# Performance work log

Measured on AMD Instinct MI355X. Metric: run time of the kernel, lower is better.

Reference implementation:

```python
import jax, jax.numpy as jnp
import numpy as np

N = 100000   # nodes
E = 600000   # edges
G = 512      # graphs in batch
EPS = 1e-5   # LayerNorm eps
IN_DIM = 60 + 2 + 12  # dyn feats*frames + dims + st embedding
H = 128


def setup_inputs() -> dict:
    key = jax.random.key(0)
    ks = jax.random.split(key, 32)
    inp = {
        "x": jax.random.normal(ks[0], (N, 60), jnp.float32),
        "xdims": jax.random.uniform(ks[1], (N, 2), jnp.float32),
        "xsttype": jax.random.randint(ks[2], (N,), 0, 256, jnp.int32),
        "edge_index": jax.random.randint(ks[3], (2, E), 0, N, jnp.int32),
        "batch": jnp.sort(jax.random.randint(ks[4], (N,), 0, G, jnp.int32)),
        "emb": jax.random.normal(ks[5], (256, 12), jnp.float32),
    }
    def lin(k, i, o):
        s = 1.0 / np.sqrt(i)
        return jax.random.uniform(k, (i, o), jnp.float32, -s, s)
    dims = [IN_DIM, H, H]
    for l in range(2):
        i, o = dims[l], dims[l + 1]
        inp[f"Wl{l}"] = lin(ks[6 + 4 * l], i, o)   # lin_l: applied to aggregated neighbors
        inp[f"bl{l}"] = jnp.zeros((o,), jnp.float32)
        inp[f"Wr{l}"] = lin(ks[7 + 4 * l], i, o)   # lin_r: applied to root (no bias, PyG SAGEConv)
        inp[f"g{l}"] = jnp.ones((o,), jnp.float32)   # LayerNorm gamma
        inp[f"bn{l}"] = jnp.zeros((o,), jnp.float32)  # LayerNorm beta
    ld = [2 * H, 50, 50, 10]
    for l in range(3):
        inp[f"Wf{l}"] = lin(ks[20 + l], ld[l], ld[l + 1])
        inp[f"bf{l}"] = jnp.zeros((ld[l + 1],), jnp.float32)
    return inp


def _layer_norm(h, g, b):
    mu = jnp.mean(h, axis=-1, keepdims=True)
    var = jnp.mean(jnp.square(h - mu), axis=-1, keepdims=True)
    return (h - mu) * jax.lax.rsqrt(var + EPS) * g + b


def reference(x, xdims, xsttype, edge_index, batch, emb,
              Wl0, bl0, Wr0, g0, bn0,
              Wl1, bl1, Wr1, g1, bn1,
              Wf0, bf0, Wf1, bf1, Wf2, bf2):
    # node feature assembly: [N, 60+2+12]
    h = jnp.concatenate([x, xdims, emb[xsttype]], axis=1)

    src, dst = edge_index[0], edge_index[1]
    deg = jax.ops.segment_sum(jnp.ones((E,), h.dtype), dst, num_segments=N)
    inv_deg = (1.0 / jnp.maximum(deg, 1.0))[:, None]

    for Wl, bl, Wr, g, bn in ((Wl0, bl0, Wr0, g0, bn0), (Wl1, bl1, Wr1, g1, bn1)):
        # SAGEConv (mean aggr): out = lin_l(mean_j x_j) + lin_r(x_i)
        agg = jax.ops.segment_sum(h[src], dst, num_segments=N) * inv_deg
        h = agg @ Wl + bl + h @ Wr
        h = jax.nn.relu(_layer_norm(h, g, bn))  # dropout inactive (eval)

    # global mean / max pooling over graphs
    cnt = jax.ops.segment_sum(jnp.ones((N,), h.dtype), batch, num_segments=G)
    xmean = jax.ops.segment_sum(h, batch, num_segments=G) / jnp.maximum(cnt, 1.0)[:, None]
    xmax = jax.ops.segment_max(h, batch, num_segments=G)
    z = jnp.concatenate([xmean, xmax], axis=1)  # [G, 2H]

    for Wf, bf in ((Wf0, bf0), (Wf1, bf1), (Wf2, bf2)):
        z = jax.nn.relu(z @ Wf + bf)  # Linear + ReLU + Dropout(eval)
    return z
```

## Files before the change

kernel.cpp:

```cpp
#include <hip/hip_runtime.h>

#define NN 100000
#define NP 100096
#define NT (NP / 32)
#define GB 1024
#define EE 600000
#define GG 512
#define LN_EPS 1e-5f

typedef __attribute__((ext_vector_type(8))) __bf16 bf16x8;
typedef __attribute__((ext_vector_type(4))) float f32x4;

__device__ __forceinline__ unsigned short f2bf(float f) {
    unsigned int u = __float_as_uint(f);
    u = (u + 0x7fffu + ((u >> 16) & 1u)) >> 16;
    return (unsigned short)u;
}
__device__ __forceinline__ unsigned int pack2(float a, float b) {
    return (unsigned int)f2bf(a) | ((unsigned int)f2bf(b) << 16);
}
__device__ __forceinline__ void acc8(float* s, uint4 v) {
    s[0] += __uint_as_float(v.x << 16);
    s[1] += __uint_as_float(v.x & 0xffff0000u);
    s[2] += __uint_as_float(v.y << 16);
    s[3] += __uint_as_float(v.y & 0xffff0000u);
    s[4] += __uint_as_float(v.z << 16);
    s[5] += __uint_as_float(v.z & 0xffff0000u);
    s[6] += __uint_as_float(v.w << 16);
    s[7] += __uint_as_float(v.w & 0xffff0000u);
}

#define PREP_A (NP * 10)
#define PREP_W0 (128 * 160)
#define PREP_W1 (128 * 256)
#define PREP_TOT (PREP_A + PREP_W0 + PREP_W1 + EE)

__global__ __launch_bounds__(256) void prep_kernel(
    const float* __restrict__ x, const float* __restrict__ xdims,
    const int* __restrict__ stt, const float* __restrict__ emb,
    const int* __restrict__ ei,
    const float* __restrict__ Wl0, const float* __restrict__ Wr0,
    const float* __restrict__ Wl1, const float* __restrict__ Wr1,
    unsigned short* __restrict__ H0r,
    unsigned short* __restrict__ Wt0, unsigned short* __restrict__ Wt1,
    int* __restrict__ deg)
{
    int idx = blockIdx.x * 256 + threadIdx.x;
    if (idx < PREP_A) {
        int node = idx / 10;
        int c8 = (idx - node * 10) * 8;
        unsigned short vals[8];
        if (node < NN) {
            int st = stt[node];
            #pragma unroll
            for (int i = 0; i < 8; ++i) {
                int f = c8 + i;
                float v = 0.f;
                if (f < 60)      v = x[node * 60 + f];
                else if (f < 62) v = xdims[node * 2 + (f - 60)];
                else if (f < 74) v = emb[st * 12 + (f - 62)];
                vals[i] = f2bf(v);
            }
        } else {
            #pragma unroll
            for (int i = 0; i < 8; ++i) vals[i] = 0;
        }
        uint4 o;
        o.x = (unsigned)vals[0] | ((unsigned)vals[1] << 16);
        o.y = (unsigned)vals[2] | ((unsigned)vals[3] << 16);
        o.z = (unsigned)vals[4] | ((unsigned)vals[5] << 16);
        o.w = (unsigned)vals[6] | ((unsigned)vals[7] << 16);
        *(uint4*)(H0r + (size_t)node * 80 + c8) = o;
    } else if (idx < PREP_A + PREP_W0) {
        int j = idx - PREP_A;
        int n = j / 160, k = j - n * 160;
        float v = 0.f;
        if (k < 74)                  v = Wl0[k * 128 + n];
        else if (k >= 80 && k < 154) v = Wr0[(k - 80) * 128 + n];
        Wt0[(size_t)n * 160 + k] = f2bf(v);
    } else if (idx < PREP_A + PREP_W0 + PREP_W1) {
        int j = idx - PREP_A - PREP_W0;
        int n = j >> 8, k = j & 255;
        float v = (k < 128) ? Wl1[k * 128 + n] : Wr1[(k - 128) * 128 + n];
        Wt1[(size_t)n * 256 + k] = f2bf(v);
    } else if (idx < PREP_TOT) {
        int e = idx - PREP_A - PREP_W0 - PREP_W1;
        atomicAdd(&deg[ei[EE + e]], 1);
    }
}

__global__ __launch_bounds__(256) void scan1_kernel(
    const int* __restrict__ deg, int* __restrict__ offs, int* __restrict__ bsum)
{
    __shared__ int ts[256];
    int t = threadIdx.x;
    int base = blockIdx.x * 2048 + t * 8;
    int d[8];
    if (base + 8 <= NN) {
        int4 a = *(const int4*)&deg[base];
        int4 b = *(const int4*)&deg[base + 4];
        d[0]=a.x; d[1]=a.y; d[2]=a.z; d[3]=a.w;
        d[4]=b.x; d[5]=b.y; d[6]=b.z; d[7]=b.w;
    } else {
        #pragma unroll
        for (int i = 0; i < 8; ++i) d[i] = (base + i < NN) ? deg[base + i] : 0;
    }
    int e[8]; int run = 0;
    #pragma unroll
    for (int i = 0; i < 8; ++i) { e[i] = run; run += d[i]; }
    ts[t] = run;
    int tot = run;
    __syncthreads();
    for (int off = 1; off < 256; off <<= 1) {
        int u = (t >= off) ? ts[t - off] : 0;
        __syncthreads();
        ts[t] += u;
        __syncthreads();
// ... 16 lines not shown
    if (t < nb) bsum[t] = inc - v;
}

__global__ __launch_bounds__(256) void fill_csr_kernel(
    const int* __restrict__ ei, int* __restrict__ cur,
    const int* __restrict__ offs, const int* __restrict__ bsum,
    int* __restrict__ csr)
{
    int e = blockIdx.x * 256 + threadIdx.x;
    if (e >= EE) return;
    int d = ei[EE + e];
    int p = offs[d] + bsum[d >> 11] + atomicAdd(&cur[d], 1);
    csr[p] = ei[e];
}

__global__ __launch_bounds__(256) void agg0_kernel(
    const unsigned short* __restrict__ H0r, unsigned short* __restrict__ A0g,
    const int* __restrict__ csr, const int* __restrict__ offs,
    const int* __restrict__ bsum, const int* __restrict__ deg)
{
    int node = blockIdx.x * 16 + (threadIdx.x >> 4);
    int lane = threadIdx.x & 15;
    if (node >= NP || lane >= 10) return;
    int d = 0, st = 0;
    if (node < NN) { d = deg[node]; st = offs[node] + bsum[node >> 11]; }
    float iv = 1.0f / (float)(d > 1 ? d : 1);
    float s[8];
    #pragma unroll
    for (int i = 0; i < 8; ++i) s[i] = 0.f;
    int e = 0;
    for (; e + 4 <= d; e += 4) {
        int i0 = csr[st + e],     i1 = csr[st + e + 1];
        int i2 = csr[st + e + 2], i3 = csr[st + e + 3];
        uint4 v0 = *(const uint4*)(H0r + (size_t)i0 * 80 + lane * 8);
        uint4 v1 = *(const uint4*)(H0r + (size_t)i1 * 80 + lane * 8);
        uint4 v2 = *(const uint4*)(H0r + (size_t)i2 * 80 + lane * 8);
        uint4 v3 = *(const uint4*)(H0r + (size_t)i3 * 80 + lane * 8);
        acc8(s, v0); acc8(s, v1); acc8(s, v2); acc8(s, v3);
    }
    for (; e < d; ++e) {
        int i0 = csr[st + e];
        uint4 v0 = *(const uint4*)(H0r + (size_t)i0 * 80 + lane * 8);
        acc8(s, v0);
    }
    uint4 o;
    o.x = pack2(s[0] * iv, s[1] * iv);
    o.y = pack2(s[2] * iv, s[3] * iv);
    o.z = pack2(s[4] * iv, s[5] * iv);
    o.w = pack2(s[6] * iv, s[7] * iv);
    *(uint4*)(A0g + (size_t)node * 80 + lane * 8) = o;
}

__global__ __launch_bounds__(256) void agg1_kernel(
    const unsigned short* __restrict__ H1, unsigned short* __restrict__ A1g,
    const int* __restrict__ csr, const int* __restrict__ offs,
    const int* __restrict__ bsum, const int* __restrict__ deg)
{
    int node = blockIdx.x * 16 + (threadIdx.x >> 4);
    int lane = threadIdx.x & 15;
    if (node >= NP) return;
    int d = 0, st = 0;
    if (node < NN) { d = deg[node]; st = offs[node] + bsum[node >> 11]; }
    float iv = 1.0f / (float)(d > 1 ? d : 1);
    float s[8];
    #pragma unroll
    for (int i = 0; i < 8; ++i) s[i] = 0.f;
    int e = 0;
    for (; e + 4 <= d; e += 4) {
        int i0 = csr[st + e],     i1 = csr[st + e + 1];
        int i2 = csr[st + e + 2], i3 = csr[st + e + 3];
        uint4 v0 = *(const uint4*)(H1 + (size_t)i0 * 128 + lane * 8);
        uint4 v1 = *(const uint4*)(H1 + (size_t)i1 * 128 + lane * 8);
        uint4 v2 = *(const uint4*)(H1 + (size_t)i2 * 128 + lane * 8);
        uint4 v3 = *(const uint4*)(H1 + (size_t)i3 * 128 + lane * 8);
        acc8(s, v0); acc8(s, v1); acc8(s, v2); acc8(s, v3);
    }
    for (; e < d; ++e) {
        int i0 = csr[st + e];
        uint4 v0 = *(const uint4*)(H1 + (size_t)i0 * 128 + lane * 8);
        acc8(s, v0);
    }
    uint4 o;
    o.x = pack2(s[0] * iv, s[1] * iv);
    o.y = pack2(s[2] * iv, s[3] * iv);
    o.z = pack2(s[4] * iv, s[5] * iv);
    o.w = pack2(s[6] * iv, s[7] * iv);
    *(uint4*)(A1g + (size_t)node * 128 + lane * 8) = o;
}

template<int K, bool POOL>
__global__ __launch_bounds__(256, 4) void gemm_kernel(
    const unsigned short* __restrict__ Ag,
    const unsigned short* __restrict__ Hr,
    const unsigned short* __restrict__ Wt,
    const float* __restrict__ bias, const float* __restrict__ gamma,
    const float* __restrict__ beta,
    unsigned short* __restrict__ outH,
    const int* __restrict__ batch,
    float* __restrict__ psum, int* __restrict__ pmax)
{
    constexpr int KT = K / 32, AS = K + 8, CPR = K / 8, CPRh = CPR / 2, RH = K / 2;
    constexpr int SMEM = (32 * AS * 2 > 32 * 128 * 4) ? 32 * AS * 2 : 32 * 128 * 4;
    __shared__ __align__(16) char smem[SMEM];
    unsigned short* Asm = (unsigned short*)smem;
    float* Hs = (float*)smem;
    __shared__ __align__(16) float sP[32 * 4];
    __shared__ __align__(16) float qP[32 * 4];
    __shared__ int bS[32];

    const int tid = threadIdx.x;
    const int l = tid & 63, w = tid >> 6;
    const int g = l >> 4, c0 = l & 15;

    bf16x8 bfr[KT][2];
    #pragma unroll
    for (int j = 0; j < 2; ++j) {
        const unsigned short* bp = Wt + (size_t)((2 * w + j) * 16 + c0) * K + g * 8;
        #pragma unroll
        for (int kt = 0; kt < KT; ++kt)
            bfr[kt][j] = *(const bf16x8*)(bp + kt * 32);
    }
    float bia[2], gam[2], bet[2];
    #pragma unroll
    for (int j = 0; j < 2; ++j) {
        int col = (2 * w + j) * 16 + c0;
        bia[j] = bias[col]; gam[j] = gamma[col]; bet[j] = beta[col];
    }
    const unsigned short* ar0 = Asm + (0 * 16 + c0) * AS + g * 8;
    const unsigned short* ar1 = Asm + (1 * 16 + c0) * AS + g * 8;

    for (int t = blockIdx.x; t < NT; t += gridDim.x) {
        const int n0 = t * 32;
        if (POOL && tid < 32) {
            int gn = n0 + tid;
            bS[tid] = (gn < NN) ? batch[gn] : -1;
        }
        for (int i = tid; i < 32 * CPR; i += 256) {
            int node = i / CPR, c = i - node * CPR;
            size_t gn = (size_t)(n0 + node);
            const unsigned short* src = (c < CPRh)
                ? (Ag + gn * RH + c * 8)
                : (Hr + gn * RH + (c - CPRh) * 8);
            uint4 v = *(const uint4*)src;
            *(uint4*)(Asm + node * AS + c * 8) = v;
        }
        __syncthreads();

        f32x4 acc[2][2];
        acc[0][0] = (f32x4){0.f,0.f,0.f,0.f}; acc[0][1] = (f32x4){0.f,0.f,0.f,0.f};
        acc[1][0] = (f32x4){0.f,0.f,0.f,0.f}; acc[1][1] = (f32x4){0.f,0.f,0.f,0.f};
        #pragma unroll
        for (int kt = 0; kt < KT; ++kt) {
            bf16x8 a0 = *(const bf16x8*)(ar0 + kt * 32);
            bf16x8 a1 = *(const bf16x8*)(ar1 + kt * 32);
            acc[0][0] = __builtin_amdgcn_mfma_f32_16x16x32_bf16(a0, bfr[kt][0], acc[0][0], 0, 0, 0);
            acc[0][1] = __builtin_amdgcn_mfma_f32_16x16x32_bf16(a0, bfr[kt][1], acc[0][1], 0, 0, 0);
            acc[1][0] = __builtin_amdgcn_mfma_f32_16x16x32_bf16(a1, bfr[kt][0], acc[1][0], 0, 0, 0);
            acc[1][1] = __builtin_amdgcn_mfma_f32_16x16x32_bf16(a1, bfr[kt][1], acc[1][1], 0, 0, 0);
        }

        #pragma unroll
        for (int m = 0; m < 2; ++m) {
            #pragma unroll
            for (int r = 0; r < 4; ++r) {
                float h0v = acc[m][0][r] + bia[0];
                float h1v = acc[m][1][r] + bia[1];
                float s = h0v + h1v, q = h0v * h0v + h1v * h1v;
                #pragma unroll
                for (int mm = 1; mm < 16; mm <<= 1) {
                    s += __shfl_xor(s, mm, 64);
                    q += __shfl_xor(q, mm, 64);
                }
                if (c0 == 0) {
                    int node = m * 16 + g * 4 + r;
                    sP[node * 4 + w] = s;
                    qP[node * 4 + w] = q;
                }
            }
        }
        __syncthreads();

        #pragma unroll
        for (int m = 0; m < 2; ++m) {
            #pragma unroll
            for (int r = 0; r < 4; ++r) {
                int node = m * 16 + g * 4 + r;
                float4 sv = *(const float4*)&sP[node * 4];
                float4 qv = *(const float4*)&qP[node * 4];
                float s = (sv.x + sv.y) + (sv.z + sv.w);
                float q = (qv.x + qv.y) + (qv.z + qv.w);
                float mu   = s * (1.f / 128.f);
                float var  = q * (1.f / 128.f) - mu * mu;
                float rinv = rsqrtf(var + LN_EPS);
                float h0v = acc[m][0][r] + bia[0];
                float h1v = acc[m][1][r] + bia[1];
                float v0 = fmaxf(0.f, (h0v - mu) * rinv * gam[0] + bet[0]);
                float v1 = fmaxf(0.f, (h1v - mu) * rinv * gam[1] + bet[1]);
                if (POOL) {
                    Hs[node * 128 + (2 * w) * 16 + c0]     = v0;
                    Hs[node * 128 + (2 * w + 1) * 16 + c0] = v1;
                } else {
                    size_t gn = (size_t)(n0 + node);
                    outH[gn * 128 + (2 * w) * 16 + c0]     = f2bf(v0);
                    outH[gn * 128 + (2 * w + 1) * 16 + c0] = f2bf(v1);
                }
            }
        }
        __syncthreads();

        if (POOL) {
            if (tid < 128) {
                int j = tid;
                int curg = -1; float s = 0.f, m = 0.f;
                #pragma unroll 4
                for (int n = 0; n < 32; ++n) {
                    int gb = bS[n];
                    if (gb < 0) break;
                    if (gb != curg) {
                        if (curg >= 0) {
                            atomicAdd(&psum[curg * 128 + j], s);
                            atomicMax(&pmax[curg * 128 + j], __float_as_int(m));
                        }
                        curg = gb; s = 0.f; m = 0.f;
                    }
                    float v = Hs[n * 128 + j];
                    s += v; m = fmaxf(m, v);
                }
                if (curg >= 0) {
                    atomicAdd(&psum[curg * 128 + j], s);
                    atomicMax(&pmax[curg * 128 + j], __float_as_int(m));
                }
            }
            __syncthreads();
        }
    }
}

__device__ __forceinline__ int lbound(const int* a, int n, int v) {
    int lo = 0, hi = n;
    while (lo < hi) { int mid = (lo + hi) >> 1; if (a[mid] < v) lo = mid + 1; else hi = mid; }
    return lo;
}

__global__ __launch_bounds__(64) void mlp_kernel(
    const float* __restrict__ psum, const int* __restrict__ pmax,
    const int* __restrict__ batch,
    const float* __restrict__ Wf0, const float* __restrict__ bf0,
    const float* __restrict__ Wf1, const float* __restrict__ bf1,
    const float* __restrict__ Wf2, const float* __restrict__ bf2,
    float* __restrict__ out)
{
    __shared__ float z[256];
    __shared__ float t1[50];
    __shared__ float t2[50];
    __shared__ int cS;
    int g = blockIdx.x, t = threadIdx.x;
    if (t == 0) cS = lbound(batch, NN, g + 1) - lbound(batch, NN, g);
    __syncthreads();
    int c = cS;
    float ic = 1.0f / (float)(c > 1 ? c : 1);
    for (int j = t; j < 128; j += 64) {
        z[j]       = psum[g * 128 + j] * ic;
        z[128 + j] = __int_as_float(pmax[g * 128 + j]);
    }
    __syncthreads();
    if (t < 50) {
// ... 13 lines not shown
        for (int k = 0; k < 50; ++k) a = fmaf(t2[k], Wf2[k * 10 + t], a);
        out[g * 10 + t] = fmaxf(a, 0.0f);
    }
}

extern "C" void kernel_launch(void* const* d_in, const int* in_sizes, int n_in,
                              void* d_out, int out_size, void* d_ws, size_t ws_size,
                              hipStream_t stream)
{
    const float* x     = (const float*)d_in[0];
    const float* xdims = (const float*)d_in[1];
    const int*   stt   = (const int*)d_in[2];
    const int*   ei    = (const int*)d_in[3];
    const int*   batch = (const int*)d_in[4];
    const float* emb   = (const float*)d_in[5];
    const float* Wl0   = (const float*)d_in[6];
    const float* bl0   = (const float*)d_in[7];
    const float* Wr0   = (const float*)d_in[8];
    const float* g0    = (const float*)d_in[9];
    const float* bn0   = (const float*)d_in[10];
    const float* Wl1   = (const float*)d_in[11];
    const float* bl1   = (const float*)d_in[12];
    const float* Wr1   = (const float*)d_in[13];
    const float* g1    = (const float*)d_in[14];
    const float* bn1   = (const float*)d_in[15];
    const float* Wf0   = (const float*)d_in[16];
    const float* bf0   = (const float*)d_in[17];
    const float* Wf1   = (const float*)d_in[18];
    const float* bf1   = (const float*)d_in[19];
    const float* Wf2   = (const float*)d_in[20];
    const float* bf2   = (const float*)d_in[21];

    char* w = (char*)d_ws;
    unsigned short* H0r = (unsigned short*)w; w += (size_t)NP * 80 * 2;
    unsigned short* A0g = (unsigned short*)w; w += (size_t)NP * 80 * 2;
    unsigned short* H1  = (unsigned short*)w; w += (size_t)NP * 128 * 2;
    unsigned short* A1g = (unsigned short*)w; w += (size_t)NP * 128 * 2;
    unsigned short* Wt0 = (unsigned short*)w; w += (size_t)128 * 160 * 2;
    unsigned short* Wt1 = (unsigned short*)w; w += (size_t)128 * 256 * 2;
    int*   csr    = (int*)w;   w += (size_t)EE * 4;
    int*   offs   = (int*)w;   w += (size_t)NN * 4;
    int*   bsum   = (int*)w;   w += 1024;
    char* zbeg = w;
    int*   deg  = (int*)w;   w += (size_t)NP * 4;
    int*   cur  = (int*)w;   w += (size_t)NN * 4;
    float* psum = (float*)w; w += (size_t)GG * 128 * 4;
    int*   pmax = (int*)w;   w += (size_t)GG * 128 * 4;
    size_t zsz = (size_t)(w - zbeg);

    hipMemsetAsync(zbeg, 0, zsz, stream);

    prep_kernel<<<(PREP_TOT + 255) / 256, 256, 0, stream>>>(
        x, xdims, stt, emb, ei, Wl0, Wr0, Wl1, Wr1, H0r, Wt0, Wt1, deg);

    int nb = (NN + 2047) / 2048;
    scan1_kernel<<<nb, 256, 0, stream>>>(deg, offs, bsum);
    scan2_kernel<<<1, 64, 0, stream>>>(bsum, nb);
    fill_csr_kernel<<<(EE + 255) / 256, 256, 0, stream>>>(ei, cur, offs, bsum, csr);

    agg0_kernel<<<NP / 16, 256, 0, stream>>>(H0r, A0g, csr, offs, bsum, deg);
    gemm_kernel<160, false><<<GB, 256, 0, stream>>>(
        A0g, H0r, Wt0, bl0, g0, bn0, H1, nullptr, nullptr, nullptr);
    agg1_kernel<<<NP / 16, 256, 0, stream>>>(H1, A1g, csr, offs, bsum, deg);
    gemm_kernel<256, true><<<GB, 256, 0, stream>>>(
        A1g, H1, Wt1, bl1, g1, bn1, nullptr, batch, psum, pmax);

    mlp_kernel<<<GG, 64, 0, stream>>>(psum, pmax, batch, Wf0, bf0, Wf1, bf1, Wf2, bf2,
                                      (float*)d_out);
}
```

Measured before the change: 329.9 us.

## Load GEMM operands directly from global memory, one 32-node tile per block

The fused SAGE GEMM+LayerNorm kernel drops its persistent-block loop and LDS staging of the activation tile. Each block now handles one 32-node tile, with every wave loading its A and W fragments straight from global memory in groups of four k-steps, then issuing the MFMAs. This removes a shared-memory round trip and a barrier per tile, and lets more blocks be resident. The cost is that each wave reloads weight fragments per tile instead of keeping them in registers across tiles, and all four waves load the same A rows redundantly.

```diff
diff --git a/kernel.cpp b/kernel.cpp
--- a/kernel.cpp
+++ b/kernel.cpp
@@ -3,7 +3,6 @@
 #define NN 100000
 #define NP 100096
 #define NT (NP / 32)
-#define GB 1024
 #define EE 600000
 #define GG 512
 #define LN_EPS 1e-5f
@@ -222,7 +221,7 @@
 }
 
 template<int K, bool POOL>
-__global__ __launch_bounds__(256, 4) void gemm_kernel(
+__global__ __launch_bounds__(256) void gemm_kernel(
     const unsigned short* __restrict__ Ag,
     const unsigned short* __restrict__ Hr,
     const unsigned short* __restrict__ Wt,
@@ -232,139 +231,139 @@
     const int* __restrict__ batch,
     float* __restrict__ psum, int* __restrict__ pmax)
 {
-    constexpr int KT = K / 32, AS = K + 8, CPR = K / 8, CPRh = CPR / 2, RH = K / 2;
-    constexpr int SMEM = (32 * AS * 2 > 32 * 128 * 4) ? 32 * AS * 2 : 32 * 128 * 4;
-    __shared__ __align__(16) char smem[SMEM];
-    unsigned short* Asm = (unsigned short*)smem;
-    float* Hs = (float*)smem;
+    constexpr int KT = K / 32, KH = K / 2;
     __shared__ __align__(16) float sP[32 * 4];
     __shared__ __align__(16) float qP[32 * 4];
-    __shared__ int bS[32];
+    __shared__ __align__(16) float Hs[POOL ? 32 * 128 : 4];
+    __shared__ int bS[POOL ? 32 : 1];
 
     const int tid = threadIdx.x;
+    const int n0 = blockIdx.x * 32;
     const int l = tid & 63, w = tid >> 6;
     const int g = l >> 4, c0 = l & 15;
 
-    bf16x8 bfr[KT][2];
-    #pragma unroll
-    for (int j = 0; j < 2; ++j) {
-        const unsigned short* bp = Wt + (size_t)((2 * w + j) * 16 + c0) * K + g * 8;
-        #pragma unroll
-        for (int kt = 0; kt < KT; ++kt)
-            bfr[kt][j] = *(const bf16x8*)(bp + kt * 32);
-    }
+    if (POOL && tid < 32) {
+        int gn = n0 + tid;
+        bS[tid] = (gn < NN) ? batch[gn] : -1;
+    }
+
+    const unsigned short* ag0 = Ag + (size_t)(n0 + c0) * KH;
+    const unsigned short* hr0 = Hr + (size_t)(n0 + c0) * KH;
+    const unsigned short* ag1 = Ag + (size_t)(n0 + 16 + c0) * KH;
+    const unsigned short* hr1 = Hr + (size_t)(n0 + 16 + c0) * KH;
+    const unsigned short* bp0 = Wt + (size_t)((2 * w + 0) * 16 + c0) * K + g * 8;
+    const unsigned short* bp1 = Wt + (size_t)((2 * w + 1) * 16 + c0) * K + g * 8;
+
     float bia[2], gam[2], bet[2];
     #pragma unroll
     for (int j = 0; j < 2; ++j) {
         int col = (2 * w + j) * 16 + c0;
         bia[j] = bias[col]; gam[j] = gamma[col]; bet[j] = beta[col];
     }
-    const unsigned short* ar0 = Asm + (0 * 16 + c0) * AS + g * 8;
-    const unsigned short* ar1 = Asm + (1 * 16 + c0) * AS + g * 8;
-
-    for (int t = blockIdx.x; t < NT; t += gridDim.x) {
-        const int n0 = t * 32;
-        if (POOL && tid < 32) {
-            int gn = n0 + tid;
-            bS[tid] = (gn < NN) ? batch[gn] : -1;
-        }
-        for (int i = tid; i < 32 * CPR; i += 256) {
-            int node = i / CPR, c = i - node * CPR;
-            size_t gn = (size_t)(n0 + node);
-            const unsigned short* src = (c < CPRh)
-                ? (Ag + gn * RH + c * 8)
-                : (Hr + gn * RH + (c - CPRh) * 8);
-            uint4 v = *(const uint4*)src;
-            *(uint4*)(Asm + node * AS + c * 8) = v;
-        }
-        __syncthreads();
-
-        f32x4 acc[2][2];
-        acc[0][0] = (f32x4){0.f,0.f,0.f,0.f}; acc[0][1] = (f32x4){0.f,0.f,0.f,0.f};
-        acc[1][0] = (f32x4){0.f,0.f,0.f,0.f}; acc[1][1] = (f32x4){0.f,0.f,0.f,0.f};
+
+    f32x4 acc[2][2];
+    acc[0][0] = (f32x4){0.f,0.f,0.f,0.f}; acc[0][1] = (f32x4){0.f,0.f,0.f,0.f};
+    acc[1][0] = (f32x4){0.f,0.f,0.f,0.f}; acc[1][1] = (f32x4){0.f,0.f,0.f,0.f};
+
+    #pragma unroll
+    for (int kb = 0; kb < KT; kb += 4) {
+        constexpr int NB = 4;
+        const int nb = (KT - kb < NB) ? (KT - kb) : NB;
+        bf16x8 bfr[NB][2], afr[NB][2];
         #pragma unroll
-        for (int kt = 0; kt < KT; ++kt) {
-            bf16x8 a0 = *(const bf16x8*)(ar0 + kt * 32);
-            bf16x8 a1 = *(const bf16x8*)(ar1 + kt * 32);
-            acc[0][0] = __builtin_amdgcn_mfma_f32_16x16x32_bf16(a0, bfr[kt][0], acc[0][0], 0, 0, 0);
-            acc[0][1] = __builtin_amdgcn_mfma_f32_16x16x32_bf16(a0, bfr[kt][1], acc[0][1], 0, 0, 0);
-            acc[1][0] = __builtin_amdgcn_mfma_f32_16x16x32_bf16(a1, bfr[kt][0], acc[1][0], 0, 0, 0);
-            acc[1][1] = __builtin_amdgcn_mfma_f32_16x16x32_bf16(a1, bfr[kt][1], acc[1][1], 0, 0, 0);
-        }
-
+        for (int kk = 0; kk < NB; ++kk) {
+            if (kk < nb) {
+                int kt = kb + kk;
+                int c = kt * 32 + g * 8;
+                bfr[kk][0] = *(const bf16x8*)(bp0 + kt * 32);
+                bfr[kk][1] = *(const bf16x8*)(bp1 + kt * 32);
+                const unsigned short* a0p = (c < KH) ? (ag0 + c) : (hr0 + c - KH);
+                const unsigned short* a1p = (c < KH) ? (ag1 + c) : (hr1 + c - KH);
+                afr[kk][0] = *(const bf16x8*)a0p;
+                afr[kk][1] = *(const bf16x8*)a1p;
+            }
+        }
         #pragma unroll
-        for (int m = 0; m < 2; ++m) {
+        for (int kk = 0; kk < NB; ++kk) {
+            if (kk < nb) {
+                acc[0][0] = __builtin_amdgcn_mfma_f32_16x16x32_bf16(afr[kk][0], bfr[kk][0], acc[0][0], 0, 0, 0);
+                acc[0][1] = __builtin_amdgcn_mfma_f32_16x16x32_bf16(afr[kk][0], bfr[kk][1], acc[0][1], 0, 0, 0);
+                acc[1][0] = __builtin_amdgcn_mfma_f32_16x16x32_bf16(afr[kk][1], bfr[kk][0], acc[1][0], 0, 0, 0);
+                acc[1][1] = __builtin_amdgcn_mfma_f32_16x16x32_bf16(afr[kk][1], bfr[kk][1], acc[1][1], 0, 0, 0);
+            }
+        }
+    }
+
+    #pragma unroll
+    for (int m = 0; m < 2; ++m) {
+        #pragma unroll
+        for (int r = 0; r < 4; ++r) {
+            float h0v = acc[m][0][r] + bia[0];
+            float h1v = acc[m][1][r] + bia[1];
+            float s = h0v + h1v, q = h0v * h0v + h1v * h1v;
             #pragma unroll
-            for (int r = 0; r < 4; ++r) {
-                float h0v = acc[m][0][r] + bia[0];
-                float h1v = acc[m][1][r] + bia[1];
-                float s = h0v + h1v, q = h0v * h0v + h1v * h1v;
-                #pragma unroll
-                for (int mm = 1; mm < 16; mm <<= 1) {
-                    s += __shfl_xor(s, mm, 64);
-                    q += __shfl_xor(q, mm, 64);
-                }
-                if (c0 == 0) {
-                    int node = m * 16 + g * 4 + r;
-                    sP[node * 4 + w] = s;
-                    qP[node * 4 + w] = q;
-                }
-            }
-        }
-        __syncthreads();
-
+            for (int mm = 1; mm < 16; mm <<= 1) {
+                s += __shfl_xor(s, mm, 64);
+                q += __shfl_xor(q, mm, 64);
+            }
+            if (c0 == 0) {
+                int node = m * 16 + g * 4 + r;
+                sP[node * 4 + w] = s;
+                qP[node * 4 + w] = q;
+            }
+        }
+    }
+    __syncthreads();
+
+    #pragma unroll
+    for (int m = 0; m < 2; ++m) {
         #pragma unroll
-        for (int m = 0; m < 2; ++m) {
-            #pragma unroll
-            for (int r = 0; r < 4; ++r) {
-                int node = m * 16 + g * 4 + r;
-                float4 sv = *(const float4*)&sP[node * 4];
-                float4 qv = *(const float4*)&qP[node * 4];
-                float s = (sv.x + sv.y) + (sv.z + sv.w);
-                float q = (qv.x + qv.y) + (qv.z + qv.w);
-                float mu   = s * (1.f / 128.f);
-                float var  = q * (1.f / 128.f) - mu * mu;
-                float rinv = rsqrtf(var + LN_EPS);
-                float h0v = acc[m][0][r] + bia[0];
-                float h1v = acc[m][1][r] + bia[1];
-                float v0 = fmaxf(0.f, (h0v - mu) * rinv * gam[0] + bet[0]);
-                float v1 = fmaxf(0.f, (h1v - mu) * rinv * gam[1] + bet[1]);
-                if (POOL) {
-                    Hs[node * 128 + (2 * w) * 16 + c0]     = v0;
-                    Hs[node * 128 + (2 * w + 1) * 16 + c0] = v1;
-                } else {
-                    size_t gn = (size_t)(n0 + node);
-                    outH[gn * 128 + (2 * w) * 16 + c0]     = f2bf(v0);
-                    outH[gn * 128 + (2 * w + 1) * 16 + c0] = f2bf(v1);
-                }
-            }
-        }
-        __syncthreads();
-
-        if (POOL) {
-            if (tid < 128) {
-                int j = tid;
-                int curg = -1; float s = 0.f, m = 0.f;
-                #pragma unroll 4
-                for (int n = 0; n < 32; ++n) {
-                    int gb = bS[n];
-                    if (gb < 0) break;
-                    if (gb != curg) {
-                        if (curg >= 0) {
-                            atomicAdd(&psum[curg * 128 + j], s);
-                            atomicMax(&pmax[curg * 128 + j], __float_as_int(m));
-                        }
-                        curg = gb; s = 0.f; m = 0.f;
-                    }
-                    float v = Hs[n * 128 + j];
-                    s += v; m = fmaxf(m, v);
-                }
+        for (int r = 0; r < 4; ++r) {
+            int node = m * 16 + g * 4 + r;
+            float4 sv = *(const float4*)&sP[node * 4];
+            float4 qv = *(const float4*)&qP[node * 4];
+            float s = (sv.x + sv.y) + (sv.z + sv.w);
+            float q = (qv.x + qv.y) + (qv.z + qv.w);
+            float mu   = s * (1.f / 128.f);
+            float var  = q * (1.f / 128.f) - mu * mu;
+            float rinv = rsqrtf(var + LN_EPS);
+            float h0v = acc[m][0][r] + bia[0];
+            float h1v = acc[m][1][r] + bia[1];
+            float v0 = fmaxf(0.f, (h0v - mu) * rinv * gam[0] + bet[0]);
+            float v1 = fmaxf(0.f, (h1v - mu) * rinv * gam[1] + bet[1]);
+            if (POOL) {
+                Hs[node * 128 + (2 * w) * 16 + c0]     = v0;
+                Hs[node * 128 + (2 * w + 1) * 16 + c0] = v1;
+            } else {
+                size_t gn = (size_t)(n0 + node);
+                outH[gn * 128 + (2 * w) * 16 + c0]     = f2bf(v0);
+                outH[gn * 128 + (2 * w + 1) * 16 + c0] = f2bf(v1);
+            }
+        }
+    }
+    if (!POOL) return;
+    __syncthreads();
+
+    if (tid < 128) {
+        int j = tid;
+        int curg = -1; float s = 0.f, m = 0.f;
+        #pragma unroll 4
+        for (int n = 0; n < 32; ++n) {
+            int gb = bS[n];
+            if (gb < 0) break;
+            if (gb != curg) {
                 if (curg >= 0) {
                     atomicAdd(&psum[curg * 128 + j], s);
                     atomicMax(&pmax[curg * 128 + j], __float_as_int(m));
                 }
-            }
-            __syncthreads();
+                curg = gb; s = 0.f; m = 0.f;
+            }
+            float v = Hs[n * 128 + j];
+            s += v; m = fmaxf(m, v);
+        }
+        if (curg >= 0) {
+            atomicAdd(&psum[curg * 128 + j], s);
+            atomicMax(&pmax[curg * 128 + j], __float_as_int(m));
         }
     }
 }
@@ -471,10 +470,10 @@
     fill_csr_kernel<<<(EE + 255) / 256, 256, 0, stream>>>(ei, cur, offs, bsum, csr);
 
     agg0_kernel<<<NP / 16, 256, 0, stream>>>(H0r, A0g, csr, offs, bsum, deg);
-    gemm_kernel<160, false><<<GB, 256, 0, stream>>>(
+    gemm_kernel<160, false><<<NT, 256, 0, stream>>>(
         A0g, H0r, Wt0, bl0, g0, bn0, H1, nullptr, nullptr, nullptr);
     agg1_kernel<<<NP / 16, 256, 0, stream>>>(H1, A1g, csr, offs, bsum, deg);
-    gemm_kernel<256, true><<<GB, 256, 0, stream>>>(
+    gemm_kernel<256, true><<<NT, 256, 0, stream>>>(
         A1g, H1, Wt1, bl1, g1, bn1, nullptr, batch, psum, pmax);
 
     mlp_kernel<<<GG, 64, 0, stream>>>(psum, pmax, batch, Wf0, bf0, Wf1, bf1, Wf2, bf2,
```

After: 325.1 us. No clear change (-1.5%).

## Restructure SAGE GEMM: direct global-to-LDS loads, 64-node tiles, padded row strides

Applied to the files above, without the earlier changes.

The GEMM kernels drop the persistent grid-stride loop over 32-node tiles. They now launch one 512-thread block per 64-node tile, and each wave computes a single 16-column slice. The A and H tiles are staged with global_load_lds straight into shared memory, skipping the register round trip. Row strides of the node feature and weight arrays are padded (88/136/168/264) so the tiles copy contiguously and LDS accesses avoid bank conflicts. In exchange, B fragments are no longer held in registers across tiles but reloaded from global memory per block. The padding also enlarges the feature buffers the aggregation kernels read and write.

```diff
diff --git a/kernel.cpp b/kernel.cpp
--- a/kernel.cpp
+++ b/kernel.cpp
@@ -2,11 +2,14 @@
 
 #define NN 100000
 #define NP 100096
-#define NT (NP / 32)
-#define GB 1024
 #define EE 600000
 #define GG 512
 #define LN_EPS 1e-5f
+
+#define PS0 88
+#define PS1 136
+#define SW0 168
+#define SW1 264
 
 typedef __attribute__((ext_vector_type(8))) __bf16 bf16x8;
 typedef __attribute__((ext_vector_type(4))) float f32x4;
@@ -28,6 +31,11 @@
     s[5] += __uint_as_float(v.z & 0xffff0000u);
     s[6] += __uint_as_float(v.w << 16);
     s[7] += __uint_as_float(v.w & 0xffff0000u);
+}
+__device__ __forceinline__ void gl_lds16(const unsigned short* g, unsigned short* l) {
+    __builtin_amdgcn_global_load_lds(
+        (const __attribute__((address_space(1))) void*)g,
+        (__attribute__((address_space(3))) void*)l, 16, 0, 0);
 }
 
 #define PREP_A (NP * 10)
@@ -70,19 +78,19 @@
         o.y = (unsigned)vals[2] | ((unsigned)vals[3] << 16);
         o.z = (unsigned)vals[4] | ((unsigned)vals[5] << 16);
         o.w = (unsigned)vals[6] | ((unsigned)vals[7] << 16);
-        *(uint4*)(H0r + (size_t)node * 80 + c8) = o;
+        *(uint4*)(H0r + (size_t)node * PS0 + c8) = o;
     } else if (idx < PREP_A + PREP_W0) {
         int j = idx - PREP_A;
         int n = j / 160, k = j - n * 160;
         float v = 0.f;
         if (k < 74)                  v = Wl0[k * 128 + n];
         else if (k >= 80 && k < 154) v = Wr0[(k - 80) * 128 + n];
-        Wt0[(size_t)n * 160 + k] = f2bf(v);
+        Wt0[(size_t)n * SW0 + k] = f2bf(v);
     } else if (idx < PREP_A + PREP_W0 + PREP_W1) {
         int j = idx - PREP_A - PREP_W0;
         int n = j >> 8, k = j & 255;
         float v = (k < 128) ? Wl1[k * 128 + n] : Wr1[(k - 128) * 128 + n];
-        Wt1[(size_t)n * 256 + k] = f2bf(v);
+        Wt1[(size_t)n * SW1 + k] = f2bf(v);
     } else if (idx < PREP_TOT) {
         int e = idx - PREP_A - PREP_W0 - PREP_W1;
         atomicAdd(&deg[ei[EE + e]], 1);
@@ -165,15 +173,15 @@
     for (; e + 4 <= d; e += 4) {
         int i0 = csr[st + e],     i1 = csr[st + e + 1];
         int i2 = csr[st + e + 2], i3 = csr[st + e + 3];
-        uint4 v0 = *(const uint4*)(H0r + (size_t)i0 * 80 + lane * 8);
-        uint4 v1 = *(const uint4*)(H0r + (size_t)i1 * 80 + lane * 8);
-        uint4 v2 = *(const uint4*)(H0r + (size_t)i2 * 80 + lane * 8);
-        uint4 v3 = *(const uint4*)(H0r + (size_t)i3 * 80 + lane * 8);
+        uint4 v0 = *(const uint4*)(H0r + (size_t)i0 * PS0 + lane * 8);
+        uint4 v1 = *(const uint4*)(H0r + (size_t)i1 * PS0 + lane * 8);
+        uint4 v2 = *(const uint4*)(H0r + (size_t)i2 * PS0 + lane * 8);
+        uint4 v3 = *(const uint4*)(H0r + (size_t)i3 * PS0 + lane * 8);
         acc8(s, v0); acc8(s, v1); acc8(s, v2); acc8(s, v3);
     }
     for (; e < d; ++e) {
         int i0 = csr[st + e];
-        uint4 v0 = *(const uint4*)(H0r + (size_t)i0 * 80 + lane * 8);
+        uint4 v0 = *(const uint4*)(H0r + (size_t)i0 * PS0 + lane * 8);
         acc8(s, v0);
     }
     uint4 o;
@@ -181,7 +189,7 @@
     o.y = pack2(s[2] * iv, s[3] * iv);
     o.z = pack2(s[4] * iv, s[5] * iv);
     o.w = pack2(s[6] * iv, s[7] * iv);
-    *(uint4*)(A0g + (size_t)node * 80 + lane * 8) = o;
+    *(uint4*)(A0g + (size_t)node * PS0 + lane * 8) = o;
 }
 
 __global__ __launch_bounds__(256) void agg1_kernel(
@@ -202,15 +210,15 @@
     for (; e + 4 <= d; e += 4) {
         int i0 = csr[st + e],     i1 = csr[st + e + 1];
         int i2 = csr[st + e + 2], i3 = csr[st + e + 3];
-        uint4 v0 = *(const uint4*)(H1 + (size_t)i0 * 128 + lane * 8);
-        uint4 v1 = *(const uint4*)(H1 + (size_t)i1 * 128 + lane * 8);
-        uint4 v2 = *(const uint4*)(H1 + (size_t)i2 * 128 + lane * 8);
-        uint4 v3 = *(const uint4*)(H1 + (size_t)i3 * 128 + lane * 8);
+        uint4 v0 = *(const uint4*)(H1 + (size_t)i0 * PS1 + lane * 8);
+        uint4 v1 = *(const uint4*)(H1 + (size_t)i1 * PS1 + lane * 8);
+        uint4 v2 = *(const uint4*)(H1 + (size_t)i2 * PS1 + lane * 8);
+        uint4 v3 = *(const uint4*)(H1 + (size_t)i3 * PS1 + lane * 8);
         acc8(s, v0); acc8(s, v1); acc8(s, v2); acc8(s, v3);
     }
     for (; e < d; ++e) {
         int i0 = csr[st + e];
-        uint4 v0 = *(const uint4*)(H1 + (size_t)i0 * 128 + lane * 8);
+        uint4 v0 = *(const uint4*)(H1 + (size_t)i0 * PS1 + lane * 8);
         acc8(s, v0);
     }
     uint4 o;
@@ -218,11 +226,11 @@
     o.y = pack2(s[2] * iv, s[3] * iv);
     o.z = pack2(s[4] * iv, s[5] * iv);
     o.w = pack2(s[6] * iv, s[7] * iv);
-    *(uint4*)(A1g + (size_t)node * 128 + lane * 8) = o;
-}
-
-template<int K, bool POOL>
-__global__ __launch_bounds__(256, 4) void gemm_kernel(
+    *(uint4*)(A1g + (size_t)node * PS1 + lane * 8) = o;
+}
+
+template<int K, int KH, int PS, int SW, bool POOL>
+__global__ __launch_bounds__(512) void gemm_kernel(
     const unsigned short* __restrict__ Ag,
     const unsigned short* __restrict__ Hr,
     const unsigned short* __restrict__ Wt,
@@ -232,139 +240,128 @@
     const int* __restrict__ batch,
     float* __restrict__ psum, int* __restrict__ pmax)
 {
-    constexpr int KT = K / 32, AS = K + 8, CPR = K / 8, CPRh = CPR / 2, RH = K / 2;
-    constexpr int SMEM = (32 * AS * 2 > 32 * 128 * 4) ? 32 * AS * 2 : 32 * 128 * 4;
-    __shared__ __align__(16) char smem[SMEM];
-    unsigned short* Asm = (unsigned short*)smem;
-    float* Hs = (float*)smem;
-    __shared__ __align__(16) float sP[32 * 4];
-    __shared__ __align__(16) float qP[32 * 4];
-    __shared__ int bS[32];
+    constexpr int KT = K / 32;
+    constexpr int CH = 64 * PS / 8;
+    __shared__ __align__(16) unsigned short ASm[2 * 64 * PS];
+    __shared__ __align__(16) float sP[64 * 8];
+    __shared__ __align__(16) float qP[64 * 8];
+    __shared__ int bS[64];
 
     const int tid = threadIdx.x;
+    const int n0 = blockIdx.x * 64;
     const int l = tid & 63, w = tid >> 6;
     const int g = l >> 4, c0 = l & 15;
 
-    bf16x8 bfr[KT][2];
-    #pragma unroll
-    for (int j = 0; j < 2; ++j) {
-        const unsigned short* bp = Wt + (size_t)((2 * w + j) * 16 + c0) * K + g * 8;
+    if (POOL && tid < 64) {
+        int gn = n0 + tid;
+        bS[tid] = (gn < NN) ? batch[gn] : -1;
+    }
+    {
+        const unsigned short* gA = Ag + (size_t)n0 * PS;
+        const unsigned short* gH = Hr + (size_t)n0 * PS;
+        for (int i = tid; i < 2 * CH; i += 512) {
+            const unsigned short* src = (i < CH) ? (gA + i * 8) : (gH + (i - CH) * 8);
+            unsigned short* dst = ASm + i * 8;
+            gl_lds16(src, dst);
+        }
+    }
+
+    const int col = w * 16 + c0;
+    const unsigned short* bp = Wt + (size_t)col * SW + g * 8;
+    const float bia = bias[col], gam = gamma[col], bet = beta[col];
+
+    __syncthreads();
+
+    f32x4 acc[4];
+    #pragma unroll
+    for (int m = 0; m < 4; ++m) acc[m] = (f32x4){0.f, 0.f, 0.f, 0.f};
+
+    #pragma unroll
+    for (int m = 0; m < 4; ++m) {
+        int node = m * 16 + c0;
+        bf16x8 af[KT], bf[KT];
+        #pragma unroll
+        for (int kt = 0; kt < KT; ++kt) {
+            int k = kt * 32 + g * 8;
+            const unsigned short* ap = (k < KH)
+                ? (ASm + node * PS + k)
+                : (ASm + 64 * PS + node * PS + (k - KH));
+            af[kt] = *(const bf16x8*)ap;
+            bf[kt] = *(const bf16x8*)(bp + kt * 32);
+        }
         #pragma unroll
         for (int kt = 0; kt < KT; ++kt)
-            bfr[kt][j] = *(const bf16x8*)(bp + kt * 32);
-    }
-    float bia[2], gam[2], bet[2];
-    #pragma unroll
-    for (int j = 0; j < 2; ++j) {
-        int col = (2 * w + j) * 16 + c0;
-        bia[j] = bias[col]; gam[j] = gamma[col]; bet[j] = beta[col];
-    }
-    const unsigned short* ar0 = Asm + (0 * 16 + c0) * AS + g * 8;
-    const unsigned short* ar1 = Asm + (1 * 16 + c0) * AS + g * 8;
-
-    for (int t = blockIdx.x; t < NT; t += gridDim.x) {
-        const int n0 = t * 32;
-        if (POOL && tid < 32) {
-            int gn = n0 + tid;
-            bS[tid] = (gn < NN) ? batch[gn] : -1;
-        }
-        for (int i = tid; i < 32 * CPR; i += 256) {
-            int node = i / CPR, c = i - node * CPR;
-            size_t gn = (size_t)(n0 + node);
-            const unsigned short* src = (c < CPRh)
-                ? (Ag + gn * RH + c * 8)
-                : (Hr + gn * RH + (c - CPRh) * 8);
-            uint4 v = *(const uint4*)src;
-            *(uint4*)(Asm + node * AS + c * 8) = v;
-        }
-        __syncthreads();
-
-        f32x4 acc[2][2];
-        acc[0][0] = (f32x4){0.f,0.f,0.f,0.f}; acc[0][1] = (f32x4){0.f,0.f,0.f,0.f};
-        acc[1][0] = (f32x4){0.f,0.f,0.f,0.f}; acc[1][1] = (f32x4){0.f,0.f,0.f,0.f};
+            acc[m] = __builtin_amdgcn_mfma_f32_16x16x32_bf16(af[kt], bf[kt], acc[m], 0, 0, 0);
+    }
+
+    #pragma unroll
+    for (int m = 0; m < 4; ++m) {
         #pragma unroll
-        for (int kt = 0; kt < KT; ++kt) {
-            bf16x8 a0 = *(const bf16x8*)(ar0 + kt * 32);
-            bf16x8 a1 = *(const bf16x8*)(ar1 + kt * 32);
-            acc[0][0] = __builtin_amdgcn_mfma_f32_16x16x32_bf16(a0, bfr[kt][0], acc[0][0], 0, 0, 0);
-            acc[0][1] = __builtin_amdgcn_mfma_f32_16x16x32_bf16(a0, bfr[kt][1], acc[0][1], 0, 0, 0);
-            acc[1][0] = __builtin_amdgcn_mfma_f32_16x16x32_bf16(a1, bfr[kt][0], acc[1][0], 0, 0, 0);
-            acc[1][1] = __builtin_amdgcn_mfma_f32_16x16x32_bf16(a1, bfr[kt][1], acc[1][1], 0, 0, 0);
-        }
-
+        for (int r = 0; r < 4; ++r) {
+            float h = acc[m][r] + bia;
+            float s = h, q = h * h;
+            #pragma unroll
+            for (int mm = 1; mm < 16; mm <<= 1) {
+                s += __shfl_xor(s, mm, 64);
+                q += __shfl_xor(q, mm, 64);
+            }
+            if (c0 == 0) {
+                int node = m * 16 + g * 4 + r;
+                sP[node * 8 + w] = s;
+                qP[node * 8 + w] = q;
+            }
+        }
+    }
+    __syncthreads();
+
+    float* Hs = (float*)ASm;
+
+    #pragma unroll
+    for (int m = 0; m < 4; ++m) {
         #pragma unroll
-        for (int m = 0; m < 2; ++m) {
-            #pragma unroll
-            for (int r = 0; r < 4; ++r) {
-                float h0v = acc[m][0][r] + bia[0];
-                float h1v = acc[m][1][r] + bia[1];
-                float s = h0v + h1v, q = h0v * h0v + h1v * h1v;
-                #pragma unroll
-                for (int mm = 1; mm < 16; mm <<= 1) {
-                    s += __shfl_xor(s, mm, 64);
-                    q += __shfl_xor(q, mm, 64);
-                }
-                if (c0 == 0) {
-                    int node = m * 16 + g * 4 + r;
-                    sP[node * 4 + w] = s;
-                    qP[node * 4 + w] = q;
-                }
+        for (int r = 0; r < 4; ++r) {
+            int node = m * 16 + g * 4 + r;
+            float4 sv0 = *(const float4*)&sP[node * 8];
+            float4 sv1 = *(const float4*)&sP[node * 8 + 4];
+            float4 qv0 = *(const float4*)&qP[node * 8];
+            float4 qv1 = *(const float4*)&qP[node * 8 + 4];
+            float s = ((sv0.x + sv0.y) + (sv0.z + sv0.w)) + ((sv1.x + sv1.y) + (sv1.z + sv1.w));
+            float q = ((qv0.x + qv0.y) + (qv0.z + qv0.w)) + ((qv1.x + qv1.y) + (qv1.z + qv1.w));
+            float mu   = s * (1.f / 128.f);
+            float var  = q * (1.f / 128.f) - mu * mu;
+            float rinv = rsqrtf(var + LN_EPS);
+            float h = acc[m][r] + bia;
+            float v = fmaxf(0.f, (h - mu) * rinv * gam + bet);
+            if (POOL) {
+                Hs[node * 128 + col] = v;
+            } else {
+                outH[(size_t)(n0 + node) * PS1 + col] = f2bf(v);
             }
         }
-        __syncthreads();
-
-        #pragma unroll
-        for (int m = 0; m < 2; ++m) {
-            #pragma unroll
-            for (int r = 0; r < 4; ++r) {
-                int node = m * 16 + g * 4 + r;
-                float4 sv = *(const float4*)&sP[node * 4];
-                float4 qv = *(const float4*)&qP[node * 4];
-                float s = (sv.x + sv.y) + (sv.z + sv.w);
-                float q = (qv.x + qv.y) + (qv.z + qv.w);
-                float mu   = s * (1.f / 128.f);
-                float var  = q * (1.f / 128.f) - mu * mu;
-                float rinv = rsqrtf(var + LN_EPS);
-                float h0v = acc[m][0][r] + bia[0];
-                float h1v = acc[m][1][r] + bia[1];
-                float v0 = fmaxf(0.f, (h0v - mu) * rinv * gam[0] + bet[0]);
-                float v1 = fmaxf(0.f, (h1v - mu) * rinv * gam[1] + bet[1]);
-                if (POOL) {
-                    Hs[node * 128 + (2 * w) * 16 + c0]     = v0;
-                    Hs[node * 128 + (2 * w + 1) * 16 + c0] = v1;
-                } else {
-                    size_t gn = (size_t)(n0 + node);
-                    outH[gn * 128 + (2 * w) * 16 + c0]     = f2bf(v0);
-                    outH[gn * 128 + (2 * w + 1) * 16 + c0] = f2bf(v1);
-                }
-            }
-        }
-        __syncthreads();
-
-        if (POOL) {
-            if (tid < 128) {
-                int j = tid;
-                int curg = -1; float s = 0.f, m = 0.f;
-                #pragma unroll 4
-                for (int n = 0; n < 32; ++n) {
-                    int gb = bS[n];
-                    if (gb < 0) break;
-                    if (gb != curg) {
-                        if (curg >= 0) {
-                            atomicAdd(&psum[curg * 128 + j], s);
-                            atomicMax(&pmax[curg * 128 + j], __float_as_int(m));
-                        }
-                        curg = gb; s = 0.f; m = 0.f;
-                    }
-                    float v = Hs[n * 128 + j];
-                    s += v; m = fmaxf(m, v);
-                }
+    }
+    if (!POOL) return;
+    __syncthreads();
+
+    if (tid < 128) {
+        int j = tid;
+        int curg = -1; float s = 0.f, m = 0.f;
+        #pragma unroll 4
+        for (int n = 0; n < 64; ++n) {
+            int gb = bS[n];
+            if (gb < 0) break;
+            if (gb != curg) {
                 if (curg >= 0) {
                     atomicAdd(&psum[curg * 128 + j], s);
                     atomicMax(&pmax[curg * 128 + j], __float_as_int(m));
                 }
+                curg = gb; s = 0.f; m = 0.f;
             }
-            __syncthreads();
+            float v = Hs[n * 128 + j];
+            s += v; m = fmaxf(m, v);
+        }
+        if (curg >= 0) {
+            atomicAdd(&psum[curg * 128 + j], s);
+            atomicMax(&pmax[curg * 128 + j], __float_as_int(m));
         }
     }
 }
@@ -444,12 +441,12 @@
     const float* bf2   = (const float*)d_in[21];
 
     char* w = (char*)d_ws;
-    unsigned short* H0r = (unsigned short*)w; w += (size_t)NP * 80 * 2;
-    unsigned short* A0g = (unsigned short*)w; w += (size_t)NP * 80 * 2;
-    unsigned short* H1  = (unsigned short*)w; w += (size_t)NP * 128 * 2;
-    unsigned short* A1g = (unsigned short*)w; w += (size_t)NP * 128 * 2;
-    unsigned short* Wt0 = (unsigned short*)w; w += (size_t)128 * 160 * 2;
-    unsigned short* Wt1 = (unsigned short*)w; w += (size_t)128 * 256 * 2;
+    unsigned short* H0r = (unsigned short*)w; w += (size_t)NP * PS0 * 2;
+    unsigned short* A0g = (unsigned short*)w; w += (size_t)NP * PS0 * 2;
+    unsigned short* H1  = (unsigned short*)w; w += (size_t)NP * PS1 * 2;
+    unsigned short* A1g = (unsigned short*)w; w += (size_t)NP * PS1 * 2;
+    unsigned short* Wt0 = (unsigned short*)w; w += (size_t)128 * SW0 * 2;
+    unsigned short* Wt1 = (unsigned short*)w; w += (size_t)128 * SW1 * 2;
     int*   csr    = (int*)w;   w += (size_t)EE * 4;
     int*   offs   = (int*)w;   w += (size_t)NN * 4;
     int*   bsum   = (int*)w;   w += 1024;
@@ -471,10 +468,10 @@
     fill_csr_kernel<<<(EE + 255) / 256, 256, 0, stream>>>(ei, cur, offs, bsum, csr);
 
     agg0_kernel<<<NP / 16, 256, 0, stream>>>(H0r, A0g, csr, offs, bsum, deg);
-    gemm_kernel<160, false><<<GB, 256, 0, stream>>>(
+    gemm_kernel<160, 80, PS0, SW0, false><<<NP / 64, 512, 0, stream>>>(
         A0g, H0r, Wt0, bl0, g0, bn0, H1, nullptr, nullptr, nullptr);
     agg1_kernel<<<NP / 16, 256, 0, stream>>>(H1, A1g, csr, offs, bsum, deg);
-    gemm_kernel<256, true><<<GB, 256, 0, stream>>>(
+    gemm_kernel<256, 128, PS1, SW1, true><<<NP / 64, 512, 0, stream>>>(
         A1g, H1, Wt1, bl1, g1, bn1, nullptr, batch, psum, pmax);
 
     mlp_kernel<<<GG, 64, 0, stream>>>(psum, pmax, batch, Wf0, bf0, Wf1, bf1, Wf2, bf2,
```

After: 355.1 us. +7.6%, slower.

## Replace persistent GEMM grid with one block per 32-node tile

Applied to the files above, without the earlier changes.

The two fused GEMM+LayerNorm kernels now launch one block per 32-node tile instead of a fixed 1024-block persistent grid that looped over tiles. Weight fragments are no longer preloaded into registers once per block. They are read from global/L2 inside the k-loop, and the A-tile load starts before the weight setup. This removes the per-tile loop and its syncs and lowers register pressure, which may let more blocks overlap. In exchange, every block re-reads the weight matrix and there are about 3128 launches' worth of block setup.

```diff
diff --git a/kernel.cpp b/kernel.cpp
--- a/kernel.cpp
+++ b/kernel.cpp
@@ -3,7 +3,6 @@
 #define NN 100000
 #define NP 100096
 #define NT (NP / 32)
-#define GB 1024
 #define EE 600000
 #define GG 512
 #define LN_EPS 1e-5f
@@ -232,139 +231,132 @@
     const int* __restrict__ batch,
     float* __restrict__ psum, int* __restrict__ pmax)
 {
-    constexpr int KT = K / 32, AS = K + 8, CPR = K / 8, CPRh = CPR / 2, RH = K / 2;
+    constexpr int KT = K / 32, AS = K + 8, CPR = K / 8, CPRh = CPR / 2, KH = K / 2;
     constexpr int SMEM = (32 * AS * 2 > 32 * 128 * 4) ? 32 * AS * 2 : 32 * 128 * 4;
     __shared__ __align__(16) char smem[SMEM];
     unsigned short* Asm = (unsigned short*)smem;
     float* Hs = (float*)smem;
     __shared__ __align__(16) float sP[32 * 4];
     __shared__ __align__(16) float qP[32 * 4];
-    __shared__ int bS[32];
+    __shared__ int bS[POOL ? 32 : 1];
 
     const int tid = threadIdx.x;
+    const int n0 = blockIdx.x * 32;
+
+    if (POOL && tid < 32) {
+        int gn = n0 + tid;
+        bS[tid] = (gn < NN) ? batch[gn] : -1;
+    }
+    for (int i = tid; i < 32 * CPR; i += 256) {
+        int node = i / CPR, c = i - node * CPR;
+        size_t gn = (size_t)(n0 + node);
+        const unsigned short* src = (c < CPRh)
+            ? (Ag + gn * KH + c * 8)
+            : (Hr + gn * KH + (c - CPRh) * 8);
+        uint4 v = *(const uint4*)src;
+        *(uint4*)(Asm + node * AS + c * 8) = v;
+    }
+
     const int l = tid & 63, w = tid >> 6;
     const int g = l >> 4, c0 = l & 15;
-
-    bf16x8 bfr[KT][2];
-    #pragma unroll
-    for (int j = 0; j < 2; ++j) {
-        const unsigned short* bp = Wt + (size_t)((2 * w + j) * 16 + c0) * K + g * 8;
-        #pragma unroll
-        for (int kt = 0; kt < KT; ++kt)
-            bfr[kt][j] = *(const bf16x8*)(bp + kt * 32);
-    }
     float bia[2], gam[2], bet[2];
     #pragma unroll
     for (int j = 0; j < 2; ++j) {
         int col = (2 * w + j) * 16 + c0;
         bia[j] = bias[col]; gam[j] = gamma[col]; bet[j] = beta[col];
     }
+    const unsigned short* bp0 = Wt + (size_t)((2 * w + 0) * 16 + c0) * K + g * 8;
+    const unsigned short* bp1 = Wt + (size_t)((2 * w + 1) * 16 + c0) * K + g * 8;
     const unsigned short* ar0 = Asm + (0 * 16 + c0) * AS + g * 8;
     const unsigned short* ar1 = Asm + (1 * 16 + c0) * AS + g * 8;
-
-    for (int t = blockIdx.x; t < NT; t += gridDim.x) {
-        const int n0 = t * 32;
-        if (POOL && tid < 32) {
-            int gn = n0 + tid;
-            bS[tid] = (gn < NN) ? batch[gn] : -1;
-        }
-        for (int i = tid; i < 32 * CPR; i += 256) {
-            int node = i / CPR, c = i - node * CPR;
-            size_t gn = (size_t)(n0 + node);
-            const unsigned short* src = (c < CPRh)
-                ? (Ag + gn * RH + c * 8)
-                : (Hr + gn * RH + (c - CPRh) * 8);
-            uint4 v = *(const uint4*)src;
-            *(uint4*)(Asm + node * AS + c * 8) = v;
-        }
-        __syncthreads();
-
-        f32x4 acc[2][2];
-        acc[0][0] = (f32x4){0.f,0.f,0.f,0.f}; acc[0][1] = (f32x4){0.f,0.f,0.f,0.f};
-        acc[1][0] = (f32x4){0.f,0.f,0.f,0.f}; acc[1][1] = (f32x4){0.f,0.f,0.f,0.f};
+    __syncthreads();
+
+    f32x4 acc[2][2];
+    acc[0][0] = (f32x4){0.f,0.f,0.f,0.f}; acc[0][1] = (f32x4){0.f,0.f,0.f,0.f};
+    acc[1][0] = (f32x4){0.f,0.f,0.f,0.f}; acc[1][1] = (f32x4){0.f,0.f,0.f,0.f};
+
+    #pragma unroll
+    for (int kt = 0; kt < KT; ++kt) {
+        bf16x8 b0 = *(const bf16x8*)(bp0 + kt * 32);
+        bf16x8 b1 = *(const bf16x8*)(bp1 + kt * 32);
+        bf16x8 a0 = *(const bf16x8*)(ar0 + kt * 32);
+        bf16x8 a1 = *(const bf16x8*)(ar1 + kt * 32);
+        acc[0][0] = __builtin_amdgcn_mfma_f32_16x16x32_bf16(a0, b0, acc[0][0], 0, 0, 0);
+        acc[0][1] = __builtin_amdgcn_mfma_f32_16x16x32_bf16(a0, b1, acc[0][1], 0, 0, 0);
+        acc[1][0] = __builtin_amdgcn_mfma_f32_16x16x32_bf16(a1, b0, acc[1][0], 0, 0, 0);
+        acc[1][1] = __builtin_amdgcn_mfma_f32_16x16x32_bf16(a1, b1, acc[1][1], 0, 0, 0);
+    }
+
+    #pragma unroll
+    for (int m = 0; m < 2; ++m) {
         #pragma unroll
-        for (int kt = 0; kt < KT; ++kt) {
-            bf16x8 a0 = *(const bf16x8*)(ar0 + kt * 32);
-            bf16x8 a1 = *(const bf16x8*)(ar1 + kt * 32);
-            acc[0][0] = __builtin_amdgcn_mfma_f32_16x16x32_bf16(a0, bfr[kt][0], acc[0][0], 0, 0, 0);
-            acc[0][1] = __builtin_amdgcn_mfma_f32_16x16x32_bf16(a0, bfr[kt][1], acc[0][1], 0, 0, 0);
-            acc[1][0] = __builtin_amdgcn_mfma_f32_16x16x32_bf16(a1, bfr[kt][0], acc[1][0], 0, 0, 0);
-            acc[1][1] = __builtin_amdgcn_mfma_f32_16x16x32_bf16(a1, bfr[kt][1], acc[1][1], 0, 0, 0);
-        }
-
-        #pragma unroll
-        for (int m = 0; m < 2; ++m) {
+        for (int r = 0; r < 4; ++r) {
+            float h0v = acc[m][0][r] + bia[0];
+            float h1v = acc[m][1][r] + bia[1];
+            float s = h0v + h1v, q = h0v * h0v + h1v * h1v;
             #pragma unroll
-            for (int r = 0; r < 4; ++r) {
-                float h0v = acc[m][0][r] + bia[0];
-                float h1v = acc[m][1][r] + bia[1];
-                float s = h0v + h1v, q = h0v * h0v + h1v * h1v;
-                #pragma unroll
-                for (int mm = 1; mm < 16; mm <<= 1) {
-                    s += __shfl_xor(s, mm, 64);
-                    q += __shfl_xor(q, mm, 64);
-                }
-                if (c0 == 0) {
-                    int node = m * 16 + g * 4 + r;
-                    sP[node * 4 + w] = s;
-                    qP[node * 4 + w] = q;
-                }
+            for (int mm = 1; mm < 16; mm <<= 1) {
+                s += __shfl_xor(s, mm, 64);
+                q += __shfl_xor(q, mm, 64);
+            }
+            if (c0 == 0) {
+                int node = m * 16 + g * 4 + r;
+                sP[node * 4 + w] = s;
+                qP[node * 4 + w] = q;
             }
         }
-        __syncthreads();
-
+    }
+    __syncthreads();
+
+    #pragma unroll
+    for (int m = 0; m < 2; ++m) {
         #pragma unroll
-        for (int m = 0; m < 2; ++m) {
-            #pragma unroll
-            for (int r = 0; r < 4; ++r) {
-                int node = m * 16 + g * 4 + r;
-                float4 sv = *(const float4*)&sP[node * 4];
-                float4 qv = *(const float4*)&qP[node * 4];
-                float s = (sv.x + sv.y) + (sv.z + sv.w);
-                float q = (qv.x + qv.y) + (qv.z + qv.w);
-                float mu   = s * (1.f / 128.f);
-                float var  = q * (1.f / 128.f) - mu * mu;
-                float rinv = rsqrtf(var + LN_EPS);
-                float h0v = acc[m][0][r] + bia[0];
-                float h1v = acc[m][1][r] + bia[1];
-                float v0 = fmaxf(0.f, (h0v - mu) * rinv * gam[0] + bet[0]);
-                float v1 = fmaxf(0.f, (h1v - mu) * rinv * gam[1] + bet[1]);
-                if (POOL) {
-                    Hs[node * 128 + (2 * w) * 16 + c0]     = v0;
-                    Hs[node * 128 + (2 * w + 1) * 16 + c0] = v1;
-                } else {
-                    size_t gn = (size_t)(n0 + node);
-                    outH[gn * 128 + (2 * w) * 16 + c0]     = f2bf(v0);
-                    outH[gn * 128 + (2 * w + 1) * 16 + c0] = f2bf(v1);
-                }
+        for (int r = 0; r < 4; ++r) {
+            int node = m * 16 + g * 4 + r;
+            float4 sv = *(const float4*)&sP[node * 4];
+            float4 qv = *(const float4*)&qP[node * 4];
+            float s = (sv.x + sv.y) + (sv.z + sv.w);
+            float q = (qv.x + qv.y) + (qv.z + qv.w);
+            float mu   = s * (1.f / 128.f);
+            float var  = q * (1.f / 128.f) - mu * mu;
+            float rinv = rsqrtf(var + LN_EPS);
+            float h0v = acc[m][0][r] + bia[0];
+            float h1v = acc[m][1][r] + bia[1];
+            float v0 = fmaxf(0.f, (h0v - mu) * rinv * gam[0] + bet[0]);
+            float v1 = fmaxf(0.f, (h1v - mu) * rinv * gam[1] + bet[1]);
+            if (POOL) {
+                Hs[node * 128 + (2 * w) * 16 + c0]     = v0;
+                Hs[node * 128 + (2 * w + 1) * 16 + c0] = v1;
+            } else {
+                size_t gn = (size_t)(n0 + node);
+                outH[gn * 128 + (2 * w) * 16 + c0]     = f2bf(v0);
+                outH[gn * 128 + (2 * w + 1) * 16 + c0] = f2bf(v1);
             }
         }
-        __syncthreads();
-
-        if (POOL) {
-            if (tid < 128) {
-                int j = tid;
-                int curg = -1; float s = 0.f, m = 0.f;
-                #pragma unroll 4
-                for (int n = 0; n < 32; ++n) {
-                    int gb = bS[n];
-                    if (gb < 0) break;
-                    if (gb != curg) {
-                        if (curg >= 0) {
-                            atomicAdd(&psum[curg * 128 + j], s);
-                            atomicMax(&pmax[curg * 128 + j], __float_as_int(m));
-                        }
-                        curg = gb; s = 0.f; m = 0.f;
-                    }
-                    float v = Hs[n * 128 + j];
-                    s += v; m = fmaxf(m, v);
-                }
+    }
+    if (!POOL) return;
+    __syncthreads();
+
+    if (tid < 128) {
+        int j = tid;
+        int curg = -1; float s = 0.f, m = 0.f;
+        #pragma unroll 4
+        for (int n = 0; n < 32; ++n) {
+            int gb = bS[n];
+            if (gb < 0) break;
+            if (gb != curg) {
                 if (curg >= 0) {
                     atomicAdd(&psum[curg * 128 + j], s);
                     atomicMax(&pmax[curg * 128 + j], __float_as_int(m));
                 }
+                curg = gb; s = 0.f; m = 0.f;
             }
-            __syncthreads();
+            float v = Hs[n * 128 + j];
+            s += v; m = fmaxf(m, v);
+        }
+        if (curg >= 0) {
+            atomicAdd(&psum[curg * 128 + j], s);
+            atomicMax(&pmax[curg * 128 + j], __float_as_int(m));
         }
     }
 }
@@ -471,10 +463,10 @@
     fill_csr_kernel<<<(EE + 255) / 256, 256, 0, stream>>>(ei, cur, offs, bsum, csr);
 
     agg0_kernel<<<NP / 16, 256, 0, stream>>>(H0r, A0g, csr, offs, bsum, deg);
-    gemm_kernel<160, false><<<GB, 256, 0, stream>>>(
+    gemm_kernel<160, false><<<NT, 256, 0, stream>>>(
         A0g, H0r, Wt0, bl0, g0, bn0, H1, nullptr, nullptr, nullptr);
     agg1_kernel<<<NP / 16, 256, 0, stream>>>(H1, A1g, csr, offs, bsum, deg);
-    gemm_kernel<256, true><<<GB, 256, 0, stream>>>(
+    gemm_kernel<256, true><<<NT, 256, 0, stream>>>(
         A1g, H1, Wt1, bl1, g1, bn1, nullptr, batch, psum, pmax);
 
     mlp_kernel<<<GG, 64, 0, stream>>>(psum, pmax, batch, Wf0, bf0, Wf1, bf1, Wf2, bf2,
```

Measured after the change: 305.3 us (median of 2 runs). 1.08x faster.
